# Optimization experiments

Hardware: AMD Instinct MI355X
Metric: run time of the kernel (lower is better)

Reference implementation:

```python
import jax, jax.numpy as jnp
import numpy as np

NUM_FRAMES = 10000
NR = 2_000_000


def _vec2skew(v):
    # Faithful to ExtrinsicsLearner.vec2skew: columns are s0,s1,s2 (stack along dim=2).
    zero = jnp.zeros_like(v[:, 0])
    s0 = jnp.stack([zero, -v[:, 2], v[:, 1]], axis=1)   # (nr, 3)
    s1 = jnp.stack([v[:, 2], zero, -v[:, 0]], axis=1)
    s2 = jnp.stack([-v[:, 1], v[:, 0], zero], axis=1)
    return jnp.stack([s0, s1, s2], axis=2)              # (nr, 3, 3)


def _exp_so3(r):
    # Rodrigues formula, matching Exp(): eps added to norm, not norm^2 clamped.
    skew = _vec2skew(r)                                  # (nr, 3, 3)
    n = jnp.linalg.norm(r, axis=1) + 1e-15               # (nr,)
    eye = jnp.eye(3, dtype=r.dtype)
    a = (jnp.sin(n) / n)[:, None, None]
    b = ((1.0 - jnp.cos(n)) / (n * n))[:, None, None]
    return eye[None] + a * skew + b * (skew @ skew)


def setup_inputs() -> dict:
    key = jax.random.key(0)
    k1, k2, k3, k4, k5 = jax.random.split(key, 5)
    # Learned per-frame pose corrections (small, as after a few optim steps)
    r = jax.random.normal(k1, (NUM_FRAMES, 3), dtype=jnp.float32) * 0.05
    t = jax.random.normal(k2, (NUM_FRAMES, 3), dtype=jnp.float32) * 0.05
    # Initial extrinsics: valid rigid transforms (R0 | t0; 0 0 0 1)
    r0 = jax.random.normal(k3, (NUM_FRAMES, 3), dtype=jnp.float32) * 0.5
    R0 = _exp_so3(r0)                                    # (N, 3, 3)
    t0 = jax.random.normal(k4, (NUM_FRAMES, 3, 1), dtype=jnp.float32)
    top = jnp.concatenate([R0, t0], axis=2)              # (N, 3, 4)
    bottom = jnp.broadcast_to(
        jnp.array([[0.0, 0.0, 0.0, 1.0]], dtype=jnp.float32), (NUM_FRAMES, 1, 4))
    initial_extrinsics = jnp.concatenate([top, bottom], axis=1)  # (N, 4, 4)
    cam_id = jax.random.randint(k5, (NR,), 0, NUM_FRAMES, dtype=jnp.int64)
    return {"r": r, "t": t, "initial_extrinsics": initial_extrinsics,
            "cam_id": cam_id}


def reference(r, t, initial_extrinsics, cam_id):
    rg = r[cam_id]                                       # (nr, 3) gather
    tg = t[cam_id]                                       # (nr, 3)
    R = _exp_so3(rg)                                     # (nr, 3, 3)
    c2w34 = jnp.concatenate([R, tg[:, :, None]], axis=2)  # (nr, 3, 4)
    bottom = jnp.broadcast_to(
        jnp.array([[0.0, 0.0, 0.0, 1.0]], dtype=c2w34.dtype), (rg.shape[0], 1, 4))
    c2w = jnp.concatenate([c2w34, bottom], axis=1)       # (nr, 4, 4)
    extrinsics = jnp.linalg.inv(c2w)                     # batched 4x4 inverse
    return initial_extrinsics[cam_id] @ extrinsics       # (nr, 4, 4)
```

## Files before the change

kernel.cpp:

```cpp
#include <hip/hip_runtime.h>

__device__ __forceinline__ void compute_M(float rx, float ry, float rz,
                                          float tx, float ty, float tz,
                                          const float* __restrict__ E,
                                          float4* __restrict__ Mout) {
    float s = rx * rx + ry * ry + rz * rz;
    float n = sqrtf(s) + 1e-15f;
    float sn = sinf(n), cn = cosf(n);
    float A = sn / n;
    float B = (1.0f - cn) / (n * n);

    float R00 = 1.0f + B * (rx * rx - s);
    float R01 =  A * rz + B * (rx * ry);
    float R02 = -A * ry + B * (rx * rz);
    float R10 = -A * rz + B * (rx * ry);
    float R11 = 1.0f + B * (ry * ry - s);
    float R12 =  A * rx + B * (ry * rz);
    float R20 =  A * ry + B * (rx * rz);
    float R21 = -A * rx + B * (ry * rz);
    float R22 = 1.0f + B * (rz * rz - s);

    float T00 = R00, T01 = R10, T02 = R20;
    float T10 = R01, T11 = R11, T12 = R21;
    float T20 = R02, T21 = R12, T22 = R22;
    float u0 = -(T00 * tx + T01 * ty + T02 * tz);
    float u1 = -(T10 * tx + T11 * ty + T12 * tz);
    float u2 = -(T20 * tx + T21 * ty + T22 * tz);

    #pragma unroll
    for (int i = 0; i < 4; ++i) {
        float e0 = E[4 * i + 0], e1 = E[4 * i + 1];
        float e2 = E[4 * i + 2], e3 = E[4 * i + 3];
        float m0 = e0 * T00 + e1 * T10 + e2 * T20;
        float m1 = e0 * T01 + e1 * T11 + e2 * T21;
        float m2 = e0 * T02 + e1 * T12 + e2 * T22;
        float m3 = e0 * u0 + e1 * u1 + e2 * u2 + e3;
        Mout[i] = make_float4(m0, m1, m2, m3);
    }
}

__global__ void build_table_kernel(const float* __restrict__ r,
                                   const float* __restrict__ t,
                                   const float* __restrict__ e0,
                                   float* __restrict__ M, int nf) {
    int f = blockIdx.x * blockDim.x + threadIdx.x;
    if (f >= nf) return;
    float4 m[4];
    compute_M(r[3 * f + 0], r[3 * f + 1], r[3 * f + 2],
              t[3 * f + 0], t[3 * f + 1], t[3 * f + 2],
              e0 + 16 * f, m);
    float4* Mo = reinterpret_cast<float4*>(M + 16 * f);
    Mo[0] = m[0]; Mo[1] = m[1]; Mo[2] = m[2]; Mo[3] = m[3];
}

__global__ void gather_kernel(const int* __restrict__ cid,
                              const float4* __restrict__ M,
                              float4* __restrict__ out, int n4) {
    int tid = blockIdx.x * blockDim.x + threadIdx.x;
    if (tid >= n4) return;
    int ray = tid >> 2;
    int c = tid & 3;
    int cam = cid[ray];
    out[tid] = M[cam * 4 + c];
}

__global__ void fused_kernel(const float* __restrict__ r,
                             const float* __restrict__ t,
                             const float* __restrict__ e0,
                             const int* __restrict__ cid,
                             float4* __restrict__ out, int nr) {
    int ray = blockIdx.x * blockDim.x + threadIdx.x;
    if (ray >= nr) return;
    int f = cid[ray];
    float4 m[4];
    compute_M(r[3 * f + 0], r[3 * f + 1], r[3 * f + 2],
              t[3 * f + 0], t[3 * f + 1], t[3 * f + 2],
              e0 + 16 * f, m);
    out[ray * 4 + 0] = m[0];
    out[ray * 4 + 1] = m[1];
    out[ray * 4 + 2] = m[2];
    out[ray * 4 + 3] = m[3];
}

extern "C" void kernel_launch(void* const* d_in, const int* in_sizes, int n_in,
                              void* d_out, int out_size, void* d_ws, size_t ws_size,
                              hipStream_t stream) {
    const float* r  = (const float*)d_in[0];
    const float* t  = (const float*)d_in[1];
    const float* e0 = (const float*)d_in[2];
    const int*  cid = (const int*)d_in[3];
    float* out = (float*)d_out;

    const int nf = in_sizes[0] / 3;
    const int nr = in_sizes[3];
    const size_t table_bytes = (size_t)nf * 16 * sizeof(float);

    if (ws_size >= table_bytes) {
        float* M = (float*)d_ws;
        {
            int threads = 256;
            int blocks = (nf + threads - 1) / threads;
            build_table_kernel<<<blocks, threads, 0, stream>>>(r, t, e0, M, nf);
        }
        {
            int n4 = nr * 4;
            int threads = 256;
            int blocks = (n4 + threads - 1) / threads;
            gather_kernel<<<blocks, threads, 0, stream>>>(
                cid, (const float4*)M, (float4*)out, n4);
        }
    } else {
        int threads = 256;
        int blocks = (nr + threads - 1) / threads;
        fused_kernel<<<blocks, threads, 0, stream>>>(
            r, t, e0, cid, (float4*)out, nr);
    }
}
```

Before: 157.2 us.

## Fuse table build and gather into one per-row kernel with nontemporal stores

Replaces the two-kernel scheme (build a per-frame 4x4 table, then gather rows per ray) with a single kernel where each thread computes one output row directly from the ray's camera parameters. This removes one kernel launch and the table write/readback, and adds nontemporal stores for the 128 MB output stream. In exchange every thread recomputes the Rodrigues rotation including sin/cos, which is four times redundant per ray and far more transcendental work than the per-frame table needed.

```diff
diff --git a/kernel.cpp b/kernel.cpp
--- a/kernel.cpp
+++ b/kernel.cpp
@@ -1,85 +1,54 @@
 #include <hip/hip_runtime.h>
 
-__device__ __forceinline__ void compute_M(float rx, float ry, float rz,
-                                          float tx, float ty, float tz,
-                                          const float* __restrict__ E,
-                                          float4* __restrict__ Mout) {
-    float s = rx * rx + ry * ry + rz * rz;
-    float n = sqrtf(s) + 1e-15f;
-    float sn = sinf(n), cn = cosf(n);
-    float A = sn / n;
-    float B = (1.0f - cn) / (n * n);
+typedef float f4 __attribute__((ext_vector_type(4)));
 
-    float R00 = 1.0f + B * (rx * rx - s);
-    float R01 =  A * rz + B * (rx * ry);
-    float R02 = -A * ry + B * (rx * rz);
-    float R10 = -A * rz + B * (rx * ry);
-    float R11 = 1.0f + B * (ry * ry - s);
-    float R12 =  A * rx + B * (ry * rz);
-    float R20 =  A * ry + B * (rx * rz);
-    float R21 = -A * rx + B * (ry * rz);
-    float R22 = 1.0f + B * (rz * rz - s);
+__global__ __launch_bounds__(256) void fused_row_kernel(
+        const float* __restrict__ r,
+        const float* __restrict__ t,
+        const float* __restrict__ e0,
+        const int* __restrict__ cid,
+        f4* __restrict__ out, int n4) {
+    const int tid = blockIdx.x * blockDim.x + threadIdx.x;
+    if (tid >= n4) return;
+    const int ray = tid >> 2;
+    const int c   = tid & 3;
+    const int f   = cid[ray];
 
-    float T00 = R00, T01 = R10, T02 = R20;
-    float T10 = R01, T11 = R11, T12 = R21;
-    float T20 = R02, T21 = R12, T22 = R22;
-    float u0 = -(T00 * tx + T01 * ty + T02 * tz);
-    float u1 = -(T10 * tx + T11 * ty + T12 * tz);
-    float u2 = -(T20 * tx + T21 * ty + T22 * tz);
+    const float rx = r[3 * f + 0], ry = r[3 * f + 1], rz = r[3 * f + 2];
+    const float tx = t[3 * f + 0], ty = t[3 * f + 1], tz = t[3 * f + 2];
 
-    #pragma unroll
-    for (int i = 0; i < 4; ++i) {
-        float e0 = E[4 * i + 0], e1 = E[4 * i + 1];
-        float e2 = E[4 * i + 2], e3 = E[4 * i + 3];
-        float m0 = e0 * T00 + e1 * T10 + e2 * T20;
-        float m1 = e0 * T01 + e1 * T11 + e2 * T21;
-        float m2 = e0 * T02 + e1 * T12 + e2 * T22;
-        float m3 = e0 * u0 + e1 * u1 + e2 * u2 + e3;
-        Mout[i] = make_float4(m0, m1, m2, m3);
-    }
-}
+    const float s = rx * rx + ry * ry + rz * rz;
+    const float n = sqrtf(s) + 1e-15f;
+    const float sn = sinf(n), cn = cosf(n);
+    const float A = sn / n;
+    const float B = (1.0f - cn) / (n * n);
 
-__global__ void build_table_kernel(const float* __restrict__ r,
-                                   const float* __restrict__ t,
-                                   const float* __restrict__ e0,
-                                   float* __restrict__ M, int nf) {
-    int f = blockIdx.x * blockDim.x + threadIdx.x;
-    if (f >= nf) return;
-    float4 m[4];
-    compute_M(r[3 * f + 0], r[3 * f + 1], r[3 * f + 2],
-              t[3 * f + 0], t[3 * f + 1], t[3 * f + 2],
-              e0 + 16 * f, m);
-    float4* Mo = reinterpret_cast<float4*>(M + 16 * f);
-    Mo[0] = m[0]; Mo[1] = m[1]; Mo[2] = m[2]; Mo[3] = m[3];
-}
+    const float R00 = 1.0f + B * (rx * rx - s);
+    const float R01 =  A * rz + B * (rx * ry);
+    const float R02 = -A * ry + B * (rx * rz);
+    const float R10 = -A * rz + B * (rx * ry);
+    const float R11 = 1.0f + B * (ry * ry - s);
+    const float R12 =  A * rx + B * (ry * rz);
+    const float R20 =  A * ry + B * (rx * rz);
+    const float R21 = -A * rx + B * (ry * rz);
+    const float R22 = 1.0f + B * (rz * rz - s);
 
-__global__ void gather_kernel(const int* __restrict__ cid,
-                              const float4* __restrict__ M,
-                              float4* __restrict__ out, int n4) {
-    int tid = blockIdx.x * blockDim.x + threadIdx.x;
-    if (tid >= n4) return;
-    int ray = tid >> 2;
-    int c = tid & 3;
-    int cam = cid[ray];
-    out[tid] = M[cam * 4 + c];
-}
+    const float T00 = R00, T01 = R10, T02 = R20;
+    const float T10 = R01, T11 = R11, T12 = R21;
+    const float T20 = R02, T21 = R12, T22 = R22;
+    const float u0 = -(T00 * tx + T01 * ty + T02 * tz);
+    const float u1 = -(T10 * tx + T11 * ty + T12 * tz);
+    const float u2 = -(T20 * tx + T21 * ty + T22 * tz);
 
-__global__ void fused_kernel(const float* __restrict__ r,
-                             const float* __restrict__ t,
-                             const float* __restrict__ e0,
-                             const int* __restrict__ cid,
-                             float4* __restrict__ out, int nr) {
-    int ray = blockIdx.x * blockDim.x + threadIdx.x;
-    if (ray >= nr) return;
-    int f = cid[ray];
-    float4 m[4];
-    compute_M(r[3 * f + 0], r[3 * f + 1], r[3 * f + 2],
-              t[3 * f + 0], t[3 * f + 1], t[3 * f + 2],
-              e0 + 16 * f, m);
-    out[ray * 4 + 0] = m[0];
-    out[ray * 4 + 1] = m[1];
-    out[ray * 4 + 2] = m[2];
-    out[ray * 4 + 3] = m[3];
+    const f4 e = *reinterpret_cast<const f4*>(e0 + 16 * f + 4 * c);
+
+    f4 m;
+    m.x = e.x * T00 + e.y * T10 + e.z * T20;
+    m.y = e.x * T01 + e.y * T11 + e.z * T21;
+    m.z = e.x * T02 + e.y * T12 + e.z * T22;
+    m.w = e.x * u0 + e.y * u1 + e.z * u2 + e.w;
+
+    __builtin_nontemporal_store(m, out + tid);
 }
 
 extern "C" void kernel_launch(void* const* d_in, const int* in_sizes, int n_in,
@@ -91,28 +60,10 @@
     const int*  cid = (const int*)d_in[3];
     float* out = (float*)d_out;
 
-    const int nf = in_sizes[0] / 3;
     const int nr = in_sizes[3];
-    const size_t table_bytes = (size_t)nf * 16 * sizeof(float);
-
-    if (ws_size >= table_bytes) {
-        float* M = (float*)d_ws;
-        {
-            int threads = 256;
-            int blocks = (nf + threads - 1) / threads;
-            build_table_kernel<<<blocks, threads, 0, stream>>>(r, t, e0, M, nf);
-        }
-        {
-            int n4 = nr * 4;
-            int threads = 256;
-            int blocks = (n4 + threads - 1) / threads;
-            gather_kernel<<<blocks, threads, 0, stream>>>(
-                cid, (const float4*)M, (float4*)out, n4);
-        }
-    } else {
-        int threads = 256;
-        int blocks = (nr + threads - 1) / threads;
-        fused_kernel<<<blocks, threads, 0, stream>>>(
-            r, t, e0, cid, (float4*)out, nr);
-    }
+    const int n4 = nr * 4;
+    const int threads = 256;
+    const int blocks = (n4 + threads - 1) / threads;
+    fused_row_kernel<<<blocks, threads, 0, stream>>>(
+        r, t, e0, cid, (f4*)out, n4);
 }
```

Result: slower. 176.1 us (+12.0%).
